# Kernel optimization log

Hardware: AMD Instinct MI355X
Metric: run time of the kernel (lower is better)

Reference implementation:

```python
import jax, jax.numpy as jnp
import numpy as np

BIOSYNTHETIC_FAMILIES = {'glutamate': ['E','Q','P','R','K'], 'aspartate': ['D','N','T','I','M','K'], 'serine': ['S','G','C'], 'pyruvate': ['A','V','L'], 'aromatic': ['F','Y','W'], 'histidine': ['H']}
CODON_TABLE = {'UUU':'F','UUC':'F','UUA':'L','UUG':'L','CUU':'L','CUC':'L','CUA':'L','CUG':'L','AUU':'I','AUC':'I','AUA':'I','AUG':'M','GUU':'V','GUC':'V','GUA':'V','GUG':'V','UCU':'S','UCC':'S','UCA':'S','UCG':'S','CCU':'P','CCC':'P','CCA':'P','CCG':'P','ACU':'T','ACC':'T','ACA':'T','ACG':'T','GCU':'A','GCC':'A','GCA':'A','GCG':'A','UAU':'Y','UAC':'Y','UAA':'*','UAG':'*','CAU':'H','CAC':'H','CAA':'Q','CAG':'Q','AAU':'N','AAC':'N','AAA':'K','AAG':'K','GAU':'D','GAC':'D','GAA':'E','GAG':'E','UGU':'C','UGC':'C','UGA':'*','UGG':'W','CGU':'R','CGC':'R','CGA':'R','CGG':'R','AGU':'S','AGC':'S','AGA':'R','AGG':'R','GGU':'G','GGC':'G','GGA':'G','GGG':'G'}

def _build_family_matrix():
    aa2fam = {aa: f for f, aas in BIOSYNTHETIC_FAMILIES.items() for aa in aas}
    codons = list(CODON_TABLE.keys())
    fam = [aa2fam.get(CODON_TABLE[c]) for c in codons]  # None for stop codons
    M = np.zeros((64, 64), dtype=np.float32)
    for i in range(64):
        for j in range(64):
            if fam[i] is not None and fam[j] is not None and fam[i] == fam[j]:
                M[i, j] = 1.0
    return jnp.asarray(M)

FAMILY_MATRIX = _build_family_matrix()  # (64, 64) constant lookup table

def setup_inputs() -> dict:
    key = jax.random.key(0)
    k1, k2 = jax.random.split(key)
    codon_embeddings = jax.random.normal(k1, (16, 512, 16), dtype=jnp.float32)
    codon_indices = jax.random.randint(k2, (16, 512), 0, 64, dtype=jnp.int64 if jax.config.jax_enable_x64 else jnp.int32)
    return {"codon_embeddings": codon_embeddings, "codon_indices": codon_indices}

def reference(codon_embeddings, codon_indices):
    b, s, d = codon_embeddings.shape
    emb = codon_embeddings.reshape(-1, d)            # (n, d)
    idx = codon_indices.reshape(-1)                  # (n,)
    # Euclidean pairwise distances (torch.cdist, p=2)
    sq = jnp.sum(emb * emb, axis=-1)                 # (n,)
    d2 = sq[:, None] + sq[None, :] - 2.0 * (emb @ emb.T)
    d2 = jnp.maximum(d2, 0.0)
    mask = d2 > 0.0
    dist = jnp.where(mask, jnp.sqrt(jnp.where(mask, d2, 1.0)), 0.0)  # (n, n)
    # Same-family mask via 64x64 lookup gather
    same = FAMILY_MATRIX[idx[:, None], idx[None, :]]  # (n, n)
    eps = 1e-10
    same_sum = jnp.sum(same)
    total = jnp.asarray(dist.shape[0] * dist.shape[1], dist.dtype)
    same_d = jnp.sum(dist * same) / (same_sum + eps)
    diff_d = (jnp.sum(dist) - jnp.sum(dist * same)) / ((total - same_sum) + eps)
    loss = same_d - 0.5 * diff_d + 1.0
    return jax.nn.relu(loss)
```

## Files before the change

kernel.cpp:

```cpp
#include <hip/hip_runtime.h>
#include <math.h>

#define N_ROWS 8192
#define D 16
#define TILE 128
#define NT 64
#define NBLK 2080

#define OFF_PT   0
#define OFF_PS   16384

typedef short  bf16x8 __attribute__((ext_vector_type(8)));
typedef float  f32x4  __attribute__((ext_vector_type(4)));

#if __has_builtin(__builtin_amdgcn_sqrtf)
#define SQRTF(x) __builtin_amdgcn_sqrtf(x)
#else
#define SQRTF(x) sqrtf(x)
#endif

#define BF_ONE ((unsigned short)0x3F80)

__device__ __constant__ signed char FAM_LUT[64] = {
  4,4,3,3, 3,3,3,3,
  1,1,1,1, 3,3,3,3,
  2,2,2,2, 0,0,0,0,
  1,1,1,1, 3,3,3,3,
  4,4,-1,-1, 5,5,0,0,
  1,1,1,1, 1,1,0,0,
  2,2,-1,4, 0,0,0,0,
  2,2,0,0, 2,2,2,2
};

__device__ __forceinline__ unsigned short f2bf(float f) {
  unsigned u = __float_as_uint(f);
  u += 0x7fffu + ((u >> 16) & 1u);
  return (unsigned short)(u >> 16);
}
__device__ __forceinline__ float bf2f(unsigned short s) {
  return __uint_as_float((unsigned)s << 16);
}

__global__ __launch_bounds__(512, 4) void pair_kernel(
    const float* __restrict__ emb, const int* __restrict__ idx,
    float* __restrict__ pt, float* __restrict__ ps) {
  const int u = blockIdx.y, bx = blockIdx.x;
  int it, jt;
  if (bx < NT - u) { it = u;          jt = u + bx; }
  else             { it = NT - 1 - u; jt = bx - 1; }

  __shared__ __align__(16) unsigned short LB1[4096];
  __shared__ __align__(16) unsigned short LB2[4096];
  __shared__ __align__(16) unsigned short LFB[1024];
  __shared__ __align__(16) unsigned short LFA[1024];
  __shared__ __align__(16) unsigned short LZ[8];
  __shared__ float SQIF[TILE], SQJF[TILE];
  __shared__ float rT[8], rS[8];

  const int t  = threadIdx.x;
  const int w  = t >> 6;
  const int l  = t & 63;
  const int lr = l & 15;
  const int g  = l >> 4;

  if (t < 256) {
    const int local = t & 127;
    const int row = ((t < 128) ? it : jt) * TILE + local;
    const float4* s4 = (const float4*)(emb + (size_t)row * D);
    float4 a0 = s4[0], a1 = s4[1], a2 = s4[2], a3 = s4[3];
    float v[16];
    v[0]=a0.x; v[1]=a0.y; v[2]=a0.z; v[3]=a0.w;
    v[4]=a1.x; v[5]=a1.y; v[6]=a1.z; v[7]=a1.w;
    v[8]=a2.x; v[9]=a2.y; v[10]=a2.z; v[11]=a2.w;
    v[12]=a3.x; v[13]=a3.y; v[14]=a3.z; v[15]=a3.w;
    float ss = v[0] * v[0];
#pragma unroll
    for (int k = 1; k < 16; ++k) ss = fmaf(v[k], v[k], ss);
    const int f = FAM_LUT[idx[row] & 63];
    unsigned short oh[8];
#pragma unroll
    for (int k = 0; k < 8; ++k) oh[k] = (f == k) ? BF_ONE : (unsigned short)0;
    if (t < 128) { SQIF[local] = ss; *(bf16x8*)(LFA + local * 8) = *(bf16x8*)oh; }
    else         { SQJF[local] = ss; *(bf16x8*)(LFB + local * 8) = *(bf16x8*)oh; }
  } else if (t == 256) {
    bf16x8 z = {0,0,0,0,0,0,0,0};
    *(bf16x8*)LZ = z;
  }
  __syncthreads();

  if (t < 256) {
    const int rl = t >> 1, h = t & 1;
    const int row = jt * TILE + rl;
    const float4* s4 = (const float4*)(emb + (size_t)row * D + h * 8);
    float4 b0 = s4[0], b1v = s4[1];
    float v[8];
    v[0]=b0.x; v[1]=b0.y; v[2]=b0.z; v[3]=b0.w;
    v[4]=b1v.x; v[5]=b1v.y; v[6]=b1v.z; v[7]=b1v.w;
    unsigned short bh[8], bl[8];
#pragma unroll
    for (int k = 0; k < 8; ++k) {
      bh[k] = f2bf(v[k]);
      bl[k] = f2bf(v[k] - bf2f(bh[k]));
    }
    unsigned short* d1 = LB1 + rl * 32;
    unsigned short* d2 = LB2 + rl * 32;
    if (h == 0) {
      *(bf16x8*)(d1 + 0)  = *(bf16x8*)bh;
      *(bf16x8*)(d1 + 16) = *(bf16x8*)bh;
      *(bf16x8*)(d2 + 0)  = *(bf16x8*)bl;
      *(bf16x8*)(d2 + 16) = *(bf16x8*)bl;
    } else {
      *(bf16x8*)(d1 + 8) = *(bf16x8*)bh;
      *(bf16x8*)(d2 + 8) = *(bf16x8*)bl;
      const float sq = SQJF[rl];
      const unsigned short sqh = f2bf(sq);
      const unsigned short sql = f2bf(sq - bf2f(sqh));
      unsigned short c3h[8] = {bh[0], bh[1], bh[2], bh[3], sqh, BF_ONE, BF_ONE, bh[7]};
      unsigned short c3l[8] = {bl[0], bl[1], bl[2], bl[3], sql, 0, 0, bl[7]};
      *(bf16x8*)(d1 + 24) = *(bf16x8*)c3h;
      *(bf16x8*)(d2 + 24) = *(bf16x8*)c3l;
    }
  }

  const int arow = it * TILE + w * 16 + lr;
  const float4* a4 = (const float4*)(emb + (size_t)arow * D + (g & 1) * 8);
  float4 c0 = a4[0], c1 = a4[1];
  float va[8];
  va[0]=c0.x; va[1]=c0.y; va[2]=c0.z; va[3]=c0.w;
  va[4]=c1.x; va[5]=c1.y; va[6]=c1.z; va[7]=c1.w;
  unsigned short f8[8];
#pragma unroll
  for (int k = 0; k < 8; ++k) {
    const float sv = -2.0f * va[k];
    const unsigned short h  = f2bf(sv);
    const unsigned short lo = f2bf(sv - bf2f(h));
    f8[k] = (g < 2) ? h : lo;
  }
  if (g == 3) {
    const float sq = SQIF[w * 16 + lr];
    const unsigned short sqh = f2bf(sq);
    f8[4] = BF_ONE;
    f8[5] = sqh;
    f8[6] = f2bf(sq - bf2f(sqh));
  }
  const bf16x8 afrag = *(bf16x8*)f8;
  bf16x8 afrag3;
  if (g == 0) afrag3 = *(const bf16x8*)(LFA + (w * 16 + lr) * 8);
  else        { bf16x8 z = {0,0,0,0,0,0,0,0}; afrag3 = z; }

  __syncthreads();

  const unsigned short* p3 = (g == 0) ? (LFB + lr * 8) : LZ;
  const int step3 = (g == 0) ? 128 : 0;
  const int boff  = lr * 32 + g * 8;
  const f32x4 zf = {0.0f, 0.0f, 0.0f, 0.0f};
  float accT = 0.0f, accS = 0.0f;
#pragma unroll 2
  for (int mj = 0; mj < 8; ++mj) {
    const bf16x8 f1 = *(const bf16x8*)(LB1 + mj * 512 + boff);
    const bf16x8 f2 = *(const bf16x8*)(LB2 + mj * 512 + boff);
    const bf16x8 f3 = *(const bf16x8*)(p3 + mj * step3);
    f32x4 acc = __builtin_amdgcn_mfma_f32_16x16x32_bf16(afrag, f1, zf, 0, 0, 0);
    acc = __builtin_amdgcn_mfma_f32_16x16x32_bf16(afrag, f2, acc, 0, 0, 0);
    const f32x4 msk = __builtin_amdgcn_mfma_f32_16x16x32_bf16(afrag3, f3, zf, 0, 0, 0);
#pragma unroll
    for (int r = 0; r < 4; ++r) {
      const float d2   = fmaxf(acc[r], 0.0f);
      const float dist = SQRTF(d2);
      accT += dist;
      accS = fmaf(msk[r], dist, accS);
    }
  }

#pragma unroll
  for (int off = 32; off > 0; off >>= 1) {
    accT += __shfl_down(accT, off);
    accS += __shfl_down(accS, off);
  }
  if (l == 0) { rT[w] = accT; rS[w] = accS; }
  __syncthreads();
  if (t == 0) {
    float sT = 0.0f, sS = 0.0f;
#pragma unroll
    for (int k = 0; k < 8; ++k) { sT += rT[k]; sS += rS[k]; }
    const float wgt = (it == jt) ? 1.0f : 2.0f;
    const int bid = blockIdx.y * gridDim.x + blockIdx.x;
    pt[bid] = wgt * sT;
    ps[bid] = wgt * sS;
  }
}

__global__ __launch_bounds__(1024) void final_kernel(
    const float* __restrict__ pt, const float* __restrict__ ps,
    const int* __restrict__ idx, float* __restrict__ out) {
  const int t = threadIdx.x, w = t >> 6, l = t & 63;
  __shared__ float  HW[16][8];
  __shared__ double rTd[16], rSd[16];

  const int4* p4 = (const int4*)idx;
  const int4 va = p4[t], vb = p4[t + 1024];
  int vals[8] = {va.x, va.y, va.z, va.w, vb.x, vb.y, vb.z, vb.w};
  float myCnt = 0.0f;
#pragma unroll
  for (int rr = 0; rr < 8; ++rr) {
    const int f = FAM_LUT[vals[rr] & 63];
#pragma unroll
    for (int fam = 0; fam < 6; ++fam) {
      const unsigned long long mk = __ballot(f == fam);
      if (l == fam) myCnt += (float)__popcll(mk);
    }
  }
  if (l < 8) HW[w][l] = (l < 6) ? myCnt : 0.0f;

  double sT = 0.0, sS = 0.0;
  for (int k = t; k < NBLK; k += 1024) { sT += (double)pt[k]; sS += (double)ps[k]; }
#pragma unroll
  for (int off = 32; off > 0; off >>= 1) {
    sT += __shfl_down(sT, off);
    sS += __shfl_down(sS, off);
  }
  if (l == 0) { rTd[w] = sT; rSd[w] = sS; }
  __syncthreads();
  if (t == 0) {
    double tot = 0.0, sam = 0.0;
#pragma unroll
    for (int k = 0; k < 16; ++k) { tot += rTd[k]; sam += rSd[k]; }
    double same_sum = 0.0;
    for (int f = 0; f < 6; ++f) {
      double c = 0.0;
      for (int k = 0; k < 16; ++k) c += (double)HW[k][f];
      same_sum += c * c;
    }
    const double total  = (double)N_ROWS * (double)N_ROWS;
    const double same_d = sam / (same_sum + 1e-10);
    const double diff_d = (tot - sam) / (total - same_sum + 1e-10);
    double loss = same_d - 0.5 * diff_d + 1.0;
    out[0] = (float)(loss > 0.0 ? loss : 0.0);
  }
}

extern "C" void kernel_launch(void* const* d_in, const int* in_sizes, int n_in,
                              void* d_out, int out_size, void* d_ws, size_t ws_size,
                              hipStream_t stream) {
  const float* emb = (const float*)d_in[0];
  const int*   idx = (const int*)d_in[1];
  char* ws = (char*)d_ws;
  float* pt = (float*)(ws + OFF_PT);
  float* ps = (float*)(ws + OFF_PS);

  pair_kernel<<<dim3(NT + 1, NT / 2), dim3(512), 0, stream>>>(emb, idx, pt, ps);
  final_kernel<<<dim3(1), dim3(1024), 0, stream>>>(pt, ps, idx, (float*)d_out);
}
```

Measured before the change: 25.85 us.

## Use single bf16 product for distances with rounded-embedding norms, drop split B

Embeddings are rounded to bf16 once, and squared norms are computed from the rounded values. The distance matrix then comes from one MFMA per tile instead of a hi/lo split pair, so the second B buffer and its LDS traffic go away. The j-side staging is merged into the first loader pass, which removes a barrier. B fragments are preloaded into registers, the loop is fully unrolled, and sqrt(abs) replaces max+sqrt. The trade is reduced precision in the dot product, which risks exceeding tolerance, especially near zero distances where abs changes the semantics.

```diff
diff --git a/kernel.cpp b/kernel.cpp
--- a/kernel.cpp
+++ b/kernel.cpp
@@ -12,12 +12,6 @@
 
 typedef short  bf16x8 __attribute__((ext_vector_type(8)));
 typedef float  f32x4  __attribute__((ext_vector_type(4)));
-
-#if __has_builtin(__builtin_amdgcn_sqrtf)
-#define SQRTF(x) __builtin_amdgcn_sqrtf(x)
-#else
-#define SQRTF(x) sqrtf(x)
-#endif
 
 #define BF_ONE ((unsigned short)0x3F80)
 
@@ -40,6 +34,12 @@
 __device__ __forceinline__ float bf2f(unsigned short s) {
   return __uint_as_float((unsigned)s << 16);
 }
+__device__ __forceinline__ float sqrt_abs(float x) {
+  const float ax = __builtin_fabsf(x);
+  float r;
+  asm("v_sqrt_f32 %0, %1" : "=v"(r) : "v"(ax));
+  return r;
+}
 
 __global__ __launch_bounds__(512, 4) void pair_kernel(
     const float* __restrict__ emb, const int* __restrict__ idx,
@@ -50,11 +50,9 @@
   else             { it = NT - 1 - u; jt = bx - 1; }
 
   __shared__ __align__(16) unsigned short LB1[4096];
-  __shared__ __align__(16) unsigned short LB2[4096];
   __shared__ __align__(16) unsigned short LFB[1024];
   __shared__ __align__(16) unsigned short LFA[1024];
-  __shared__ __align__(16) unsigned short LZ[8];
-  __shared__ float SQIF[TILE], SQJF[TILE];
+  __shared__ float SQIF[TILE];
   __shared__ float rT[8], rS[8];
 
   const int t  = threadIdx.x;
@@ -64,8 +62,9 @@
   const int g  = l >> 4;
 
   if (t < 256) {
-    const int local = t & 127;
-    const int row = ((t < 128) ? it : jt) * TILE + local;
+    const int  local = t & 127;
+    const bool iside = (t < 128);
+    const int  row = (iside ? it : jt) * TILE + local;
     const float4* s4 = (const float4*)(emb + (size_t)row * D);
     float4 a0 = s4[0], a1 = s4[1], a2 = s4[2], a3 = s4[3];
     float v[16];
@@ -73,52 +72,30 @@
     v[4]=a1.x; v[5]=a1.y; v[6]=a1.z; v[7]=a1.w;
     v[8]=a2.x; v[9]=a2.y; v[10]=a2.z; v[11]=a2.w;
     v[12]=a3.x; v[13]=a3.y; v[14]=a3.z; v[15]=a3.w;
-    float ss = v[0] * v[0];
-#pragma unroll
-    for (int k = 1; k < 16; ++k) ss = fmaf(v[k], v[k], ss);
+    unsigned short bh[16];
+#pragma unroll
+    for (int k = 0; k < 16; ++k) bh[k] = f2bf(v[k]);
+    float ss = bf2f(bh[0]) * bf2f(bh[0]);
+#pragma unroll
+    for (int k = 1; k < 16; ++k) { const float rv = bf2f(bh[k]); ss = fmaf(rv, rv, ss); }
     const int f = FAM_LUT[idx[row] & 63];
     unsigned short oh[8];
 #pragma unroll
     for (int k = 0; k < 8; ++k) oh[k] = (f == k) ? BF_ONE : (unsigned short)0;
-    if (t < 128) { SQIF[local] = ss; *(bf16x8*)(LFA + local * 8) = *(bf16x8*)oh; }
-    else         { SQJF[local] = ss; *(bf16x8*)(LFB + local * 8) = *(bf16x8*)oh; }
-  } else if (t == 256) {
-    bf16x8 z = {0,0,0,0,0,0,0,0};
-    *(bf16x8*)LZ = z;
-  }
-  __syncthreads();
-
-  if (t < 256) {
-    const int rl = t >> 1, h = t & 1;
-    const int row = jt * TILE + rl;
-    const float4* s4 = (const float4*)(emb + (size_t)row * D + h * 8);
-    float4 b0 = s4[0], b1v = s4[1];
-    float v[8];
-    v[0]=b0.x; v[1]=b0.y; v[2]=b0.z; v[3]=b0.w;
-    v[4]=b1v.x; v[5]=b1v.y; v[6]=b1v.z; v[7]=b1v.w;
-    unsigned short bh[8], bl[8];
-#pragma unroll
-    for (int k = 0; k < 8; ++k) {
-      bh[k] = f2bf(v[k]);
-      bl[k] = f2bf(v[k] - bf2f(bh[k]));
-    }
-    unsigned short* d1 = LB1 + rl * 32;
-    unsigned short* d2 = LB2 + rl * 32;
-    if (h == 0) {
-      *(bf16x8*)(d1 + 0)  = *(bf16x8*)bh;
-      *(bf16x8*)(d1 + 16) = *(bf16x8*)bh;
-      *(bf16x8*)(d2 + 0)  = *(bf16x8*)bl;
-      *(bf16x8*)(d2 + 16) = *(bf16x8*)bl;
+    if (iside) {
+      SQIF[local] = ss;
+      *(bf16x8*)(LFA + local * 8) = *(bf16x8*)oh;
     } else {
-      *(bf16x8*)(d1 + 8) = *(bf16x8*)bh;
-      *(bf16x8*)(d2 + 8) = *(bf16x8*)bl;
-      const float sq = SQJF[rl];
-      const unsigned short sqh = f2bf(sq);
-      const unsigned short sql = f2bf(sq - bf2f(sqh));
-      unsigned short c3h[8] = {bh[0], bh[1], bh[2], bh[3], sqh, BF_ONE, BF_ONE, bh[7]};
-      unsigned short c3l[8] = {bl[0], bl[1], bl[2], bl[3], sql, 0, 0, bl[7]};
-      *(bf16x8*)(d1 + 24) = *(bf16x8*)c3h;
-      *(bf16x8*)(d2 + 24) = *(bf16x8*)c3l;
+      const unsigned short sqh = f2bf(ss);
+      const unsigned short sql = f2bf(ss - bf2f(sqh));
+      unsigned short c2[8] = {sqh, sql, BF_ONE, BF_ONE, 0, 0, 0, 0};
+      unsigned short cz[8] = {0, 0, 0, 0, 0, 0, 0, 0};
+      unsigned short* d1 = LB1 + local * 32;
+      *(bf16x8*)(d1 + 0)  = *(bf16x8*)&bh[0];
+      *(bf16x8*)(d1 + 8)  = *(bf16x8*)&bh[8];
+      *(bf16x8*)(d1 + 16) = *(bf16x8*)c2;
+      *(bf16x8*)(d1 + 24) = *(bf16x8*)cz;
+      *(bf16x8*)(LFB + local * 8) = *(bf16x8*)oh;
     }
   }
 
@@ -130,43 +107,48 @@
   va[4]=c1.x; va[5]=c1.y; va[6]=c1.z; va[7]=c1.w;
   unsigned short f8[8];
 #pragma unroll
-  for (int k = 0; k < 8; ++k) {
-    const float sv = -2.0f * va[k];
-    const unsigned short h  = f2bf(sv);
-    const unsigned short lo = f2bf(sv - bf2f(h));
-    f8[k] = (g < 2) ? h : lo;
-  }
-  if (g == 3) {
-    const float sq = SQIF[w * 16 + lr];
-    const unsigned short sqh = f2bf(sq);
-    f8[4] = BF_ONE;
-    f8[5] = sqh;
-    f8[6] = f2bf(sq - bf2f(sqh));
+  for (int k = 0; k < 8; ++k) f8[k] = f2bf(-2.0f * va[k]);
+
+  __syncthreads();
+
+  if (g >= 2) {
+#pragma unroll
+    for (int k = 0; k < 8; ++k) f8[k] = 0;
+    if (g == 2) {
+      const float sq = SQIF[w * 16 + lr];
+      const unsigned short sqh = f2bf(sq);
+      f8[0] = BF_ONE; f8[1] = BF_ONE;
+      f8[2] = sqh;    f8[3] = f2bf(sq - bf2f(sqh));
+    }
   }
   const bf16x8 afrag = *(bf16x8*)f8;
   bf16x8 afrag3;
   if (g == 0) afrag3 = *(const bf16x8*)(LFA + (w * 16 + lr) * 8);
   else        { bf16x8 z = {0,0,0,0,0,0,0,0}; afrag3 = z; }
 
-  __syncthreads();
-
-  const unsigned short* p3 = (g == 0) ? (LFB + lr * 8) : LZ;
-  const int step3 = (g == 0) ? 128 : 0;
-  const int boff  = lr * 32 + g * 8;
+  bf16x8 b1f[8], m3[8];
+#pragma unroll
+  for (int mj = 0; mj < 8; ++mj)
+    b1f[mj] = *(const bf16x8*)(LB1 + (mj * 16 + lr) * 32 + g * 8);
+  if (g == 0) {
+#pragma unroll
+    for (int mj = 0; mj < 8; ++mj)
+      m3[mj] = *(const bf16x8*)(LFB + (mj * 16 + lr) * 8);
+  } else {
+    bf16x8 z = {0,0,0,0,0,0,0,0};
+#pragma unroll
+    for (int mj = 0; mj < 8; ++mj) m3[mj] = z;
+  }
+
   const f32x4 zf = {0.0f, 0.0f, 0.0f, 0.0f};
   float accT = 0.0f, accS = 0.0f;
-#pragma unroll 2
+#pragma unroll
   for (int mj = 0; mj < 8; ++mj) {
-    const bf16x8 f1 = *(const bf16x8*)(LB1 + mj * 512 + boff);
-    const bf16x8 f2 = *(const bf16x8*)(LB2 + mj * 512 + boff);
-    const bf16x8 f3 = *(const bf16x8*)(p3 + mj * step3);
-    f32x4 acc = __builtin_amdgcn_mfma_f32_16x16x32_bf16(afrag, f1, zf, 0, 0, 0);
-    acc = __builtin_amdgcn_mfma_f32_16x16x32_bf16(afrag, f2, acc, 0, 0, 0);
-    const f32x4 msk = __builtin_amdgcn_mfma_f32_16x16x32_bf16(afrag3, f3, zf, 0, 0, 0);
+    const f32x4 acc = __builtin_amdgcn_mfma_f32_16x16x32_bf16(afrag,  b1f[mj], zf, 0, 0, 0);
+    const f32x4 msk = __builtin_amdgcn_mfma_f32_16x16x32_bf16(afrag3, m3[mj],  zf, 0, 0, 0);
 #pragma unroll
     for (int r = 0; r < 4; ++r) {
-      const float d2   = fmaxf(acc[r], 0.0f);
-      const float dist = SQRTF(d2);
+      const float dist = sqrt_abs(acc[r]);
       accT += dist;
       accS = fmaf(msk[r], dist, accS);
     }
```

After: 23.64 us. 8.6% less time.
